# Performance work log

Measured on AMD Instinct MI355X. Metric: run time of the kernel, lower is better.

Reference implementation:

```python
import jax, jax.numpy as jnp
import numpy as np

N, E, D = 100000, 640000, 128


def _xavier(key, shape):
    return jax.random.normal(key, shape, jnp.float32) * np.float32(np.sqrt(2.0 / (shape[0] + shape[1])))


def setup_inputs() -> dict:
    key = jax.random.key(0)
    ks = jax.random.split(key, 16)
    inp = {
        "x": jax.random.normal(ks[0], (N, D), jnp.float32),
        "prompt_h": jax.random.normal(ks[1], (N, D), jnp.float32),
        "edge_attr": jax.random.normal(ks[2], (E, D), jnp.float32),
        "prompt_e": jax.random.normal(ks[3], (E, D), jnp.float32),
        "edge_index": jax.random.randint(ks[4], (2, E), 0, N, dtype=jnp.int32),
        # Linear weights stored [in, out] (torch stores [out, in]; math identical)
        "Wq": _xavier(ks[5], (D, D)), "bq": jnp.zeros((D,), jnp.float32),
        "Wk": _xavier(ks[6], (D, D)), "bk": jnp.zeros((D,), jnp.float32),
        "Wv": _xavier(ks[7], (D, D)), "bv": jnp.zeros((D,), jnp.float32),
        "We1": _xavier(ks[8], (D, D)), "be1": jnp.zeros((D,), jnp.float32),
        "We2": _xavier(ks[9], (D, D)), "be2": jnp.zeros((D,), jnp.float32),
        "Wh": _xavier(ks[10], (D, D)), "bh": jnp.zeros((D,), jnp.float32),
        "Wf1": _xavier(ks[11], (D, 2 * D)), "bf1": jnp.zeros((2 * D,), jnp.float32),
        "Wf2": _xavier(ks[12], (2 * D, D)), "bf2": jnp.zeros((D,), jnp.float32),
    }
    return inp


def reference(x, prompt_h, edge_attr, prompt_e, edge_index,
              Wq, bq, Wk, bk, Wv, bv, We1, be1, We2, be2,
              Wh, bh, Wf1, bf1, Wf2, bf2):
    relu = jax.nn.relu
    # Projections (dropout=0, eval mode)
    Q = x @ Wq + bq                      # [N, D]
    K = prompt_h @ Wk + bk               # [N, D]
    V = prompt_h @ Wv + bv               # [N, D]
    h = relu(Q * K)                      # attn_product='mul', score_act with relu
    # Edge-enhanced messages: gather source node scores per edge
    src = h[edge_index[0]]               # [E, D]
    e = relu((edge_attr + prompt_e) @ We1 + be1)
    e = relu((e + prompt_e) @ We2 + be2)  # updated edge_attr (update_e=True)
    msg = relu(src + e)                  # [E, D]
    # scatter-add aggregation into destination nodes
    aggr = jax.ops.segment_sum(msg, edge_index[1], num_segments=x.shape[0])  # [N, D]
    h_out = relu((h + V + aggr) @ Wh + bh)
    h_out = h_out + x                    # residual (in_dim == out_dim)
    h_out = relu(h_out @ Wf1 + bf1)
    h_out = h_out @ Wf2 + bf2            # [N, D]
    return h_out, e
```

## Files before the change

### kernel.cpp

```cpp
#include <hip/hip_runtime.h>

typedef __attribute__((ext_vector_type(8))) short bfrag;
typedef __attribute__((ext_vector_type(4))) float f4;

__device__ __forceinline__ unsigned short f2b(float f) {
  unsigned int u = __builtin_bit_cast(unsigned int, f);
  u = (u + 0x7fffu + ((u >> 16) & 1u)) >> 16;
  return (unsigned short)u;
}
__device__ __forceinline__ float b2f(unsigned short s) {
  unsigned int u = ((unsigned int)s) << 16;
  return __builtin_bit_cast(float, u);
}
__device__ __forceinline__ float relu(float v) { return v > 0.f ? v : 0.f; }

__device__ __forceinline__ void stage_A(char* dst, const float* s0, long r0, long maxRow) {
  const int tid = threadIdx.x;
#pragma unroll
  for (int i = 0; i < 4; ++i) {
    int ch = tid + (i << 8);
    int row = ch >> 4, kg = ch & 15;
    long gr = r0 + row;
    float v[8];
    if (gr < maxRow) {
      const float4* p = (const float4*)(s0 + gr * 128 + kg * 8);
      float4 a = p[0], b = p[1];
      v[0] = a.x; v[1] = a.y; v[2] = a.z; v[3] = a.w;
      v[4] = b.x; v[5] = b.y; v[6] = b.z; v[7] = b.w;
    } else {
#pragma unroll
      for (int j = 0; j < 8; ++j) v[j] = 0.f;
    }
    union { unsigned short h[8]; uint4 u; } pk;
#pragma unroll
    for (int j = 0; j < 8; ++j) pk.h[j] = f2b(v[j]);
    *(uint4*)(dst + (((row << 8) + (kg << 4)) ^ ((row & 7) << 4))) = pk.u;
  }
}

__device__ __forceinline__ void stage_A_mix(char* dst, const unsigned short* hb,
                                            const float* ag, long r0, long maxRow) {
  const int tid = threadIdx.x;
#pragma unroll
  for (int i = 0; i < 4; ++i) {
    int ch = tid + (i << 8);
    int row = ch >> 4, kg = ch & 15;
    long gr = r0 + row;
    union { unsigned short h[8]; uint4 u; } pk;
    if (gr < maxRow) {
      uint4 hv = *(const uint4*)(hb + gr * 128 + kg * 8);
      const float4* q = (const float4*)(ag + gr * 128 + kg * 8);
      float4 c = q[0], d = q[1];
      pk.h[0] = f2b(b2f((unsigned short)hv.x) + c.x);
      pk.h[1] = f2b(b2f((unsigned short)(hv.x >> 16)) + c.y);
      pk.h[2] = f2b(b2f((unsigned short)hv.y) + c.z);
      pk.h[3] = f2b(b2f((unsigned short)(hv.y >> 16)) + c.w);
      pk.h[4] = f2b(b2f((unsigned short)hv.z) + d.x);
      pk.h[5] = f2b(b2f((unsigned short)(hv.z >> 16)) + d.y);
      pk.h[6] = f2b(b2f((unsigned short)hv.w) + d.z);
      pk.h[7] = f2b(b2f((unsigned short)(hv.w >> 16)) + d.w);
    } else {
      pk.u = uint4{0, 0, 0, 0};
    }
    *(uint4*)(dst + (((row << 8) + (kg << 4)) ^ ((row & 7) << 4))) = pk.u;
  }
}

__device__ __forceinline__ void stage_W(char* dst, const unsigned short* src,
                                        int rowStride, int kOff) {
  const int tid = threadIdx.x;
#pragma unroll
  for (int i = 0; i < 8; ++i) {
    int ch = tid + (i << 8);
    int col = ch >> 4, kg = ch & 15;
    uint4 u = *(const uint4*)(src + (size_t)col * rowStride + kOff + kg * 8);
    *(uint4*)(dst + (((col << 8) + (kg << 4)) ^ ((col & 7) << 4))) = u;
  }
}

__device__ __forceinline__ void stage_Wh(char* dst, const unsigned short* src,
                                         int rowStride, int kOff) {
  const int tid = threadIdx.x;
#pragma unroll
  for (int i = 0; i < 4; ++i) {
    int ch = tid + (i << 8);
    int c = ch >> 3, kg = ch & 7;
    uint4 u = *(const uint4*)(src + (size_t)c * rowStride + kOff + kg * 8);
    *(uint4*)(dst + (((c << 7) + (kg << 4)) ^ ((c & 7) << 4))) = u;
  }
}

__device__ __forceinline__ void mm(const char* A, const char* W, int wm, int wn,
                                   int lane, f4 acc[2][4]) {
#pragma unroll
  for (int kk = 0; kk < 4; ++kk) {
    bfrag a[2], b[4];
#pragma unroll
    for (int rt = 0; rt < 2; ++rt) {
      int row = (wm << 5) + (rt << 4) + (lane & 15);
      a[rt] = *(const bfrag*)(A + (((row << 8) + (kk << 6) + ((lane >> 4) << 4)) ^ ((row & 7) << 4)));
    }
#pragma unroll
    for (int ct = 0; ct < 4; ++ct) {
      int col = (wn << 6) + (ct << 4) + (lane & 15);
      b[ct] = *(const bfrag*)(W + (((col << 8) + (kk << 6) + ((lane >> 4) << 4)) ^ ((col & 7) << 4)));
    }
#pragma unroll
    for (int rt = 0; rt < 2; ++rt)
#pragma unroll
      for (int ct = 0; ct < 4; ++ct)
        acc[rt][ct] = __builtin_amdgcn_mfma_f32_16x16x32_bf16(a[rt], b[ct], acc[rt][ct], 0, 0, 0);
  }
}

__device__ __forceinline__ void mm_h(const char* A, const char* W, int wm, int wn,
                                     int lane, f4 acc[2][4], int kh) {
#pragma unroll
  for (int kk2 = 0; kk2 < 2; ++kk2) {
    int kA = (kh << 1) + kk2;
    bfrag a[2], b[4];
#pragma unroll
    for (int rt = 0; rt < 2; ++rt) {
      int row = (wm << 5) + (rt << 4) + (lane & 15);
      a[rt] = *(const bfrag*)(A + (((row << 8) + (kA << 6) + ((lane >> 4) << 4)) ^ ((row & 7) << 4)));
    }
#pragma unroll
    for (int ct = 0; ct < 4; ++ct) {
      int col = (wn << 6) + (ct << 4) + (lane & 15);
      b[ct] = *(const bfrag*)(W + (((col << 7) + (kk2 << 6) + ((lane >> 4) << 4)) ^ ((col & 7) << 4)));
    }
#pragma unroll
    for (int rt = 0; rt < 2; ++rt)
#pragma unroll
      for (int ct = 0; ct < 4; ++ct)
        acc[rt][ct] = __builtin_amdgcn_mfma_f32_16x16x32_bf16(a[rt], b[ct], acc[rt][ct], 0, 0, 0);
  }
}

__device__ __forceinline__ void dump_half(char* Wl, const f4 acc[2][4], int lane, int wn) {
#pragma unroll
  for (int ct = 0; ct < 4; ++ct) {
    int col = (wn << 6) + (ct << 4) + (lane & 15);
#pragma unroll
    for (int rt = 0; rt < 2; ++rt)
#pragma unroll
      for (int j = 0; j < 4; ++j) {
        int lr = (rt << 4) + ((lane >> 4) << 2) + j;
        *(float*)(Wl + (((lr << 9) + (col << 2)) ^ ((lr & 7) << 4))) = acc[rt][ct][j];
      }
  }
}

__device__ __forceinline__ void dump_full(char* stg, const f4 acc[2][4], int lane, int wm, int wn) {
#pragma unroll
  for (int ct = 0; ct < 4; ++ct) {
    int col = (wn << 6) + (ct << 4) + (lane & 15);
#pragma unroll
    for (int rt = 0; rt < 2; ++rt)
#pragma unroll
      for (int j = 0; j < 4; ++j) {
        int rl = (wm << 5) + (rt << 4) + ((lane >> 4) << 2) + j;
        *(float*)(stg + (((rl << 9) + (col << 2)) ^ ((rl & 7) << 4))) = acc[rt][ct][j];
      }
  }
}

__global__ void k_prep(const float* __restrict__ Wq, const float* __restrict__ Wk,
                       const float* __restrict__ Wv, const float* __restrict__ We1,
                       const float* __restrict__ We2, const float* __restrict__ Wh,
                       const float* __restrict__ Wf1, const float* __restrict__ Wf2,
                       unsigned short* __restrict__ wt) {
  int b = blockIdx.x, t = threadIdx.x;
  if (b < 384) {
    int m = b >> 6;
    const float* tbl[6] = {Wq, Wk, Wv, We1, We2, Wh};
    const float* src = tbl[m];
    int local = ((b & 63) << 8) + t;
    int n = local >> 7, k = local & 127;
    wt[m * 16384 + local] = f2b(src[k * 128 + n]);
  } else if (b < 512) {
    int local = ((b - 384) << 8) + t;
    int n = local >> 7, k = local & 127;
    wt[98304 + local] = f2b(Wf1[k * 256 + n]);
  } else {
    int local = ((b - 512) << 8) + t;
    int n = local >> 8, k = local & 255;
    wt[131072 + local] = f2b(Wf2[k * 128 + n]);
  }
}

__global__ void k_deg(const int* __restrict__ ei, int* __restrict__ deg, long E) {
  long g = (long)blockIdx.x * 256 + threadIdx.x;
  if (g < E) atomicAdd(deg + ei[E + g], 1);
}

__global__ void k_scanA(const int* __restrict__ deg, int* __restrict__ ex,
                        int* __restrict__ bsum, int n) {
  __shared__ int s[256];
  int t = threadIdx.x; int g = blockIdx.x * 256 + t;
  int v = (g < n) ? deg[g] : 0;
  int val = v;
  s[t] = val; __syncthreads();
#pragma unroll
  for (int o = 1; o < 256; o <<= 1) {
    int u = (t >= o) ? s[t - o] : 0;
    __syncthreads();
    val += u; s[t] = val;
    __syncthreads();
  }
  if (g < n) ex[g] = val - v;
  if (t == 255) bsum[blockIdx.x] = val;
}

__global__ void k_scanB(int* __restrict__ bsum, int nb) {
  __shared__ int s[1024];
  int t = threadIdx.x;
  int v = (t < nb) ? bsum[t] : 0;
  int val = v;
  s[t] = val; __syncthreads();
#pragma unroll
  for (int o = 1; o < 1024; o <<= 1) {
    int u = (t >= o) ? s[t - o] : 0;
    __syncthreads();
    val += u; s[t] = val;
    __syncthreads();
  }
  if (t < nb) bsum[t] = val - v;
}

__global__ void k_scanC(const int* __restrict__ ex, const int* __restrict__ bsum,
                        int* __restrict__ off, int* __restrict__ cursor, int n) {
  int g = blockIdx.x * 256 + threadIdx.x;
  if (g < n) {
    int o = ex[g] + bsum[blockIdx.x];
    off[g] = o; cursor[g] = o;
  }
}

__global__ void k_fill(const int* __restrict__ ei, int* __restrict__ cursor,
                       int* __restrict__ eidx, long E) {
  long g = (long)blockIdx.x * 256 + threadIdx.x;
  if (g < E) {
    int pos = atomicAdd(cursor + ei[E + g], 1);
    eidx[pos] = (int)g;
  }
}

__global__ __launch_bounds__(256, 2) void k_nodes1(
    const float* __restrict__ x, const float* __restrict__ ph,
    const float* __restrict__ bq, const float* __restrict__ bk,
    const float* __restrict__ bv, const unsigned short* __restrict__ wt,
    unsigned short* __restrict__ hbf, unsigned short* __restrict__ hpvb, long N) {
  extern __shared__ char sm[];
  char* Ax = sm;
  char* Aph = sm + 16384;
  char* Wl = sm + 32768;
  long n0 = (long)blockIdx.x * 64;
  const int tid = threadIdx.x, lane = tid & 63, w = tid >> 6, wm = w >> 1, wn = w & 1;
  const int team = tid >> 5, c0 = (tid & 31) << 2;
  stage_A(Ax, x, n0, N);
  stage_A(Aph, ph, n0, N);
  stage_W(Wl, wt + 0, 128, 0);
  __syncthreads();
  f4 accQ[2][4] = {};
  mm(Ax, Wl, wm, wn, lane, accQ);
  __syncthreads();
  stage_W(Wl, wt + 16384, 128, 0);
  __syncthreads();
  f4 accK[2][4] = {};
  mm(Aph, Wl, wm, wn, lane, accK);
  __syncthreads();
  stage_W(Wl, wt + 32768, 128, 0);
  __syncthreads();
  f4 accV[2][4] = {};
  mm(Aph, Wl, wm, wn, lane, accV);
  __syncthreads();
#pragma unroll
  for (int ct = 0; ct < 4; ++ct) {
    int col = (wn << 6) + (ct << 4) + (lane & 15);
    float vbq = bq[col], vbk = bk[col], vbv = bv[col];
#pragma unroll
    for (int rt = 0; rt < 2; ++rt)
#pragma unroll
      for (int j = 0; j < 4; ++j) {
        int rl = (wm << 5) + (rt << 4) + ((lane >> 4) << 2) + j;
        float q = accQ[rt][ct][j] + vbq;
        float k = accK[rt][ct][j] + vbk;
        float v = accV[rt][ct][j] + vbv;
        float h = relu(q * k);
        *(unsigned short*)(Ax + (((rl << 8) + (col << 1)) ^ ((rl & 7) << 4))) = f2b(h);
        *(unsigned short*)(Aph + (((rl << 8) + (col << 1)) ^ ((rl & 7) << 4))) = f2b(h + v);
      }
  }
  __syncthreads();
#pragma unroll
  for (int it = 0; it < 8; ++it) {
    int r = team + (it << 3);
    long row = n0 + r;
    if (row < N) {
      uint2 hb = *(const uint2*)(Ax + (((r << 8) + (c0 << 1)) ^ ((r & 7) << 4)));
      uint2 hv = *(const uint2*)(Aph + (((r << 8) + (c0 << 1)) ^ ((r & 7) << 4)));
      *(uint2*)(hbf + row * 128 + c0) = hb;
      *(uint2*)(hpvb + row * 128 + c0) = hv;
    }
  }
}

__global__ __launch_bounds__(256, 3) void k_edges(
    const float* __restrict__ ea, const float* __restrict__ pe,
    const float* __restrict__ be1, const float* __restrict__ be2,
    const unsigned short* __restrict__ wt, const int* __restrict__ ei,
    const unsigned short* __restrict__ hbf, unsigned short* __restrict__ msg,
    float* __restrict__ eout, long E) {
  extern __shared__ char sm[];
  char* A = sm;
  unsigned short* peL = (unsigned short*)(sm + 16384);
  char* Wl = sm + 32768;
  char* stg = sm + 16384;
  const int tid = threadIdx.x;
  const int team = tid >> 5, c0 = (tid & 31) << 2;
  long e0 = (long)blockIdx.x * 64;

  uint2 hu[8];
#pragma unroll
  for (int it = 0; it < 8; ++it) {
    int r = team + (it << 3);
    long ge = e0 + r;
    int s = (ge < E) ? ei[ge] : 0;
    hu[it] = *(const uint2*)(hbf + (long)s * 128 + c0);
  }
#pragma unroll
  for (int i = 0; i < 4; ++i) {
    int ch = tid + (i << 8);
    int row = ch >> 4, kg = ch & 15;
    long gr = e0 + row;
    union { unsigned short h[8]; uint4 u; } s, q;
    if (gr < E) {
      const float4* pa = (const float4*)(ea + gr * 128 + kg * 8);
      const float4* pp = (const float4*)(pe + gr * 128 + kg * 8);
      float4 a0 = pa[0], a1 = pa[1];
      float4 p0 = pp[0], p1 = pp[1];
      s.h[0] = f2b(a0.x + p0.x); s.h[1] = f2b(a0.y + p0.y);
      s.h[2] = f2b(a0.z + p0.z); s.h[3] = f2b(a0.w + p0.w);
      s.h[4] = f2b(a1.x + p1.x); s.h[5] = f2b(a1.y + p1.y);
      s.h[6] = f2b(a1.z + p1.z); s.h[7] = f2b(a1.w + p1.w);
      q.h[0] = f2b(p0.x); q.h[1] = f2b(p0.y); q.h[2] = f2b(p0.z); q.h[3] = f2b(p0.w);
      q.h[4] = f2b(p1.x); q.h[5] = f2b(p1.y); q.h[6] = f2b(p1.z); q.h[7] = f2b(p1.w);
    } else {
      s.u = uint4{0, 0, 0, 0}; q.u = uint4{0, 0, 0, 0};
    }
    *(uint4*)((char*)peL + (row << 8) + (kg << 4)) = q.u;
    *(uint4*)(A + (((row << 8) + (kg << 4)) ^ ((row & 7) << 4))) = s.u;
  }
  stage_Wh(Wl, wt + 49152, 128, 0);
  __syncthreads();
  const int lane = tid & 63, w = tid >> 6, wm = w >> 1, wn = w & 1;
  f4 acc[2][4] = {};
  mm_h(A, Wl, wm, wn, lane, acc, 0);
  __syncthreads();
  stage_Wh(Wl, wt + 49152, 128, 64);
  __syncthreads();
  mm_h(A, Wl, wm, wn, lane, acc, 1);
  __syncthreads();
  const float4 vb1 = *(const float4*)(be1 + c0);
#pragma unroll
  for (int h = 0; h < 2; ++h) {
    if (wm == h) dump_half(Wl, acc, lane, wn);
    __syncthreads();
#pragma unroll
    for (int it = 0; it < 4; ++it) {
      int lr = team + (it << 3);
      int r = (h << 5) + lr;
      f4 a = *(const f4*)(Wl + (((lr << 9) + (c0 << 2)) ^ ((lr & 7) << 4)));
      uint2 pu = *(const uint2*)(peL + (r << 7) + c0);
      float p0 = b2f((unsigned short)pu.x), p1 = b2f((unsigned short)(pu.x >> 16));
      float p2 = b2f((unsigned short)pu.y), p3 = b2f((unsigned short)(pu.y >> 16));
      unsigned short t0 = f2b(relu(a[0] + vb1.x) + p0);
      unsigned short t1 = f2b(relu(a[1] + vb1.y) + p1);
      unsigned short t2 = f2b(relu(a[2] + vb1.z) + p2);
      unsigned short t3 = f2b(relu(a[3] + vb1.w) + p3);
      uint2 op;
      op.x = (unsigned int)t0 | ((unsigned int)t1 << 16);
      op.y = (unsigned int)t2 | ((unsigned int)t3 << 16);
      *(uint2*)(A + (((r << 8) + (c0 << 1)) ^ ((r & 7) << 4))) = op;
    }
    __syncthreads();
  }
  stage_Wh(Wl, wt + 65536, 128, 0);
  __syncthreads();
  f4 acc2[2][4] = {};
  mm_h(A, Wl, wm, wn, lane, acc2, 0);
  __syncthreads();
  stage_Wh(Wl, wt + 65536, 128, 64);
  __syncthreads();
  mm_h(A, Wl, wm, wn, lane, acc2, 1);
  __syncthreads();
  dump_full(stg, acc2, lane, wm, wn);
  __syncthreads();
  const float4 vb2 = *(const float4*)(be2 + c0);
#pragma unroll
  for (int it = 0; it < 8; ++it) {
    int r = team + (it << 3);
    long edge = e0 + r;
    if (edge < E) {
      f4 a = *(const f4*)(stg + (((r << 9) + (c0 << 2)) ^ ((r & 7) << 4)));
      float ev0 = relu(a[0] + vb2.x), ev1 = relu(a[1] + vb2.y);
      float ev2 = relu(a[2] + vb2.z), ev3 = relu(a[3] + vb2.w);
      float4 ov; ov.x = ev0; ov.y = ev1; ov.z = ev2; ov.w = ev3;
      *(float4*)(eout + edge * 128 + c0) = ov;
      float h0 = b2f((unsigned short)hu[it].x), h1 = b2f((unsigned short)(hu[it].x >> 16));
      float h2 = b2f((unsigned short)hu[it].y), h3 = b2f((unsigned short)(hu[it].y >> 16));
      unsigned short m0 = f2b(relu(ev0 + h0)), m1 = f2b(relu(ev1 + h1));
      unsigned short m2 = f2b(relu(ev2 + h2)), m3 = f2b(relu(ev3 + h3));
      uint2 mo;
      mo.x = (unsigned int)m0 | ((unsigned int)m1 << 16);
      mo.y = (unsigned int)m2 | ((unsigned int)m3 << 16);
      *(uint2*)(msg + edge * 128 + c0) = mo;
    }
  }
}

__global__ __launch_bounds__(256) void k_aggr(
    const int* __restrict__ off, const int* __restrict__ deg,
    const int* __restrict__ eidx, const unsigned short* __restrict__ msg,
    float* __restrict__ aggr, long N) {
  long node = (long)blockIdx.x * 4 + (threadIdx.x >> 6);
  if (node >= N) return;
  const int lane = threadIdx.x & 63;
  int st = off[node], d = deg[node];
  float a0 = 0.f, a1 = 0.f;
  int i = 0;
  for (; i + 3 < d; i += 4) {
    int e0i = eidx[st + i], e1i = eidx[st + i + 1];
    int e2i = eidx[st + i + 2], e3i = eidx[st + i + 3];
    unsigned int u0 = *(const unsigned int*)(msg + (long)e0i * 128 + lane * 2);
    unsigned int u1 = *(const unsigned int*)(msg + (long)e1i * 128 + lane * 2);
    unsigned int u2 = *(const unsigned int*)(msg + (long)e2i * 128 + lane * 2);
    unsigned int u3 = *(const unsigned int*)(msg + (long)e3i * 128 + lane * 2);
    a0 += b2f((unsigned short)u0) + b2f((unsigned short)u1) +
          b2f((unsigned short)u2) + b2f((unsigned short)u3);
    a1 += b2f((unsigned short)(u0 >> 16)) + b2f((unsigned short)(u1 >> 16)) +
          b2f((unsigned short)(u2 >> 16)) + b2f((unsigned short)(u3 >> 16));
  }
  for (; i < d; ++i) {
    int eid = eidx[st + i];
    unsigned int u = *(const unsigned int*)(msg + (long)eid * 128 + lane * 2);
    a0 += b2f((unsigned short)u);
    a1 += b2f((unsigned short)(u >> 16));
  }
  *(float2*)(aggr + node * 128 + lane * 2) = float2{a0, a1};
}

__global__ __launch_bounds__(256, 2) void k_nodes2(
    const unsigned short* __restrict__ hpvb, const float* __restrict__ aggr,
    const float* __restrict__ x, const float* __restrict__ bh,
    const float* __restrict__ bf1, const float* __restrict__ bf2,
    const unsigned short* __restrict__ wt, float* __restrict__ out, long N) {
  extern __shared__ char sm[];
  char* A = sm;
  char* T = sm + 16384;
  char* Wl = sm + 32768;
  long n0 = (long)blockIdx.x * 64;
  const int tid = threadIdx.x;
  stage_A_mix(A, hpvb, aggr, n0, N);
  stage_W(Wl, wt + 81920, 128, 0);
  __syncthreads();
  const int lane = tid & 63, w = tid >> 6, wm = w >> 1, wn = w & 1;
  f4 acc1[2][4] = {};
  mm(A, Wl, wm, wn, lane, acc1);
  __syncthreads();
#pragma unroll
  for (int ct = 0; ct < 4; ++ct) {
    int col = (wn << 6) + (ct << 4) + (lane & 15);
    float bb = bh[col];
#pragma unroll
    for (int rt = 0; rt < 2; ++rt)
#pragma unroll
      for (int j = 0; j < 4; ++j) {
        int rl = (wm << 5) + (rt << 4) + ((lane >> 4) << 2) + j;
        long row = n0 + rl;
        float xv = (row < N) ? x[row * 128 + col] : 0.f;
        float tv = relu(acc1[rt][ct][j] + bb) + xv;
        *(unsigned short*)(T + (((rl << 8) + (col << 1)) ^ ((rl & 7) << 4))) = f2b(tv);
      }
  }
  stage_W(Wl, wt + 98304, 128, 0);
  __syncthreads();
  f4 accA[2][4] = {};
  mm(T, Wl, wm, wn, lane, accA);
  __syncthreads();
#pragma unroll
  for (int ct = 0; ct < 4; ++ct) {
    int col = (wn << 6) + (ct << 4) + (lane & 15);
    float bb = bf1[col];
#pragma unroll
    for (int rt = 0; rt < 2; ++rt)
#pragma unroll
      for (int j = 0; j < 4; ++j) {
        int rl = (wm << 5) + (rt << 4) + ((lane >> 4) << 2) + j;
        float uv = relu(accA[rt][ct][j] + bb);
        *(unsigned short*)(A + (((rl << 8) + (col << 1)) ^ ((rl & 7) << 4))) = f2b(uv);
      }
  }
  stage_W(Wl, wt + 131072, 256, 0);
  __syncthreads();
  f4 acc3[2][4] = {};
  mm(A, Wl, wm, wn, lane, acc3);
  __syncthreads();
  stage_W(Wl, wt + 114688, 128, 0);
  __syncthreads();
  f4 accB[2][4] = {};
  mm(T, Wl, wm, wn, lane, accB);
  __syncthreads();
#pragma unroll
  for (int ct = 0; ct < 4; ++ct) {
    int col = (wn << 6) + (ct << 4) + (lane & 15);
    float bb = bf1[128 + col];
#pragma unroll
    for (int rt = 0; rt < 2; ++rt)
#pragma unroll
      for (int j = 0; j < 4; ++j) {
        int rl = (wm << 5) + (rt << 4) + ((lane >> 4) << 2) + j;
        float uv = relu(accB[rt][ct][j] + bb);
        *(unsigned short*)(A + (((rl << 8) + (col << 1)) ^ ((rl & 7) << 4))) = f2b(uv);
      }
  }
  stage_W(Wl, wt + 131072, 256, 128);
  __syncthreads();
  mm(A, Wl, wm, wn, lane, acc3);
#pragma unroll
  for (int ct = 0; ct < 4; ++ct) {
    int col = (wn << 6) + (ct << 4) + (lane & 15);
    float bb = bf2[col];
#pragma unroll
    for (int rt = 0; rt < 2; ++rt)
#pragma unroll
      for (int j = 0; j < 4; ++j) {
        int rl = (wm << 5) + (rt << 4) + ((lane >> 4) << 2) + j;
        long row = n0 + rl;
        if (row < N) out[row * 128 + col] = acc3[rt][ct][j] + bb;
      }
  }
}

extern "C" void kernel_launch(void* const* d_in, const int* in_sizes, int n_in,
                              void* d_out, int out_size, void* d_ws, size_t ws_size,
                              hipStream_t stream) {
  const float* x   = (const float*)d_in[0];
  const float* ph  = (const float*)d_in[1];
  const float* ea  = (const float*)d_in[2];
  const float* pe  = (const float*)d_in[3];
  const int*   ei  = (const int*)d_in[4];
  const float* Wq  = (const float*)d_in[5];  const float* bq  = (const float*)d_in[6];
  const float* Wk  = (const float*)d_in[7];  const float* bk  = (const float*)d_in[8];
  const float* Wv  = (const float*)d_in[9];  const float* bv  = (const float*)d_in[10];
  const float* We1 = (const float*)d_in[11]; const float* be1 = (const float*)d_in[12];
  const float* We2 = (const float*)d_in[13]; const float* be2 = (const float*)d_in[14];
  const float* Wh  = (const float*)d_in[15]; const float* bh  = (const float*)d_in[16];
  const float* Wf1 = (const float*)d_in[17]; const float* bf1 = (const float*)d_in[18];
  const float* Wf2 = (const float*)d_in[19]; const float* bf2 = (const float*)d_in[20];
  const long N = in_sizes[0] / 128;
  const long E = in_sizes[2] / 128;

  char* ws = (char*)d_ws;
  size_t pos_ = 0;
  auto alloc = [&](size_t bytes) { size_t p = pos_; pos_ += (bytes + 255) & ~255ULL; return p; };
  size_t o_wt   = alloc(327680);
  size_t o_hbf  = alloc((size_t)N * 256);
  size_t o_hpv  = alloc((size_t)N * 256);
  size_t o_aggr = alloc((size_t)N * 512);
  size_t o_deg  = alloc((size_t)N * 4);
  size_t o_ex   = alloc((size_t)N * 4);
  size_t o_cur  = alloc((size_t)N * 4);
  size_t o_off  = alloc((size_t)N * 4);
  size_t o_bsum = alloc(4096);
  size_t o_eidx = alloc((size_t)E * 4);
  size_t o_msg  = alloc((size_t)E * 256);
  (void)pos_;

  unsigned short* wt   = (unsigned short*)(ws + o_wt);
  unsigned short* hbf  = (unsigned short*)(ws + o_hbf);
  unsigned short* hpvb = (unsigned short*)(ws + o_hpv);
  float* aggr = (float*)(ws + o_aggr);
  float* outH = (float*)d_out;
  float* outE = outH + N * 128;

  k_prep<<<640, 256, 0, stream>>>(Wq, Wk, Wv, We1, We2, Wh, Wf1, Wf2, wt);
  int nb = (int)((N + 63) / 64);
  int eb = (int)((E + 63) / 64);
  k_nodes1<<<nb, 256, 65536, stream>>>(x, ph, bq, bk, bv, wt, hbf, hpvb, N);

  int* deg = (int*)(ws + o_deg);
  int* ex  = (int*)(ws + o_ex);
  int* cur = (int*)(ws + o_cur);
  int* off = (int*)(ws + o_off);
  int* bsum = (int*)(ws + o_bsum);
  int* eidx = (int*)(ws + o_eidx);
  unsigned short* msg = (unsigned short*)(ws + o_msg);
  int nb1 = (int)((N + 255) / 256);
  hipMemsetAsync(deg, 0, (size_t)N * 4, stream);
  k_deg<<<(int)((E + 255) / 256), 256, 0, stream>>>(ei, deg, E);
  k_scanA<<<nb1, 256, 0, stream>>>(deg, ex, bsum, (int)N);
  k_scanB<<<1, 1024, 0, stream>>>(bsum, nb1);
  k_scanC<<<nb1, 256, 0, stream>>>(ex, bsum, off, cur, (int)N);
  k_fill<<<(int)((E + 255) / 256), 256, 0, stream>>>(ei, cur, eidx, E);
  k_edges<<<eb, 256, 49152, stream>>>(ea, pe, be1, be2, wt, ei, hbf, msg, outE, E);
  k_aggr<<<(int)((N + 3) / 4), 256, 0, stream>>>(off, deg, eidx, msg, aggr, N);
  k_nodes2<<<nb, 256, 65536, stream>>>(hpvb, aggr, x, bh, bf1, bf2, wt, outH, N);
}
```

Baseline: 582.4 us.

## Fuse CSR aggregation into node MLP kernel and defer source-row gather in edge kernel

Removes the separate k_aggr kernel and its fp32 aggr buffer. k_nodes2 now gathers messages per destination node directly into its shared-memory A tile, adding the h+V term before bf16 packing. The residual x is prestaged into shared memory as bf16 instead of read from global in the epilogue. In k_edges, source indices go to shared memory and the hbf gather moves to the epilogue instead of being held in registers across the GEMMs. This lowers register pressure and global traffic, but the fused gather may serialize latency inside the GEMM kernel, and x is now rounded to bf16.

Result: no change. 591.6 us (+1.6%).

```diff
diff --git a/kernel.cpp b/kernel.cpp
--- a/kernel.cpp
+++ b/kernel.cpp
@@ -34,34 +34,6 @@
     union { unsigned short h[8]; uint4 u; } pk;
 #pragma unroll
     for (int j = 0; j < 8; ++j) pk.h[j] = f2b(v[j]);
-    *(uint4*)(dst + (((row << 8) + (kg << 4)) ^ ((row & 7) << 4))) = pk.u;
-  }
-}
-
-__device__ __forceinline__ void stage_A_mix(char* dst, const unsigned short* hb,
-                                            const float* ag, long r0, long maxRow) {
-  const int tid = threadIdx.x;
-#pragma unroll
-  for (int i = 0; i < 4; ++i) {
-    int ch = tid + (i << 8);
-    int row = ch >> 4, kg = ch & 15;
-    long gr = r0 + row;
-    union { unsigned short h[8]; uint4 u; } pk;
-    if (gr < maxRow) {
-      uint4 hv = *(const uint4*)(hb + gr * 128 + kg * 8);
-      const float4* q = (const float4*)(ag + gr * 128 + kg * 8);
-      float4 c = q[0], d = q[1];
-      pk.h[0] = f2b(b2f((unsigned short)hv.x) + c.x);
-      pk.h[1] = f2b(b2f((unsigned short)(hv.x >> 16)) + c.y);
-      pk.h[2] = f2b(b2f((unsigned short)hv.y) + c.z);
-      pk.h[3] = f2b(b2f((unsigned short)(hv.y >> 16)) + c.w);
-      pk.h[4] = f2b(b2f((unsigned short)hv.z) + d.x);
-      pk.h[5] = f2b(b2f((unsigned short)(hv.z >> 16)) + d.y);
-      pk.h[6] = f2b(b2f((unsigned short)hv.w) + d.z);
-      pk.h[7] = f2b(b2f((unsigned short)(hv.w >> 16)) + d.w);
-    } else {
-      pk.u = uint4{0, 0, 0, 0};
-    }
     *(uint4*)(dst + (((row << 8) + (kg << 4)) ^ ((row & 7) << 4))) = pk.u;
   }
 }
@@ -317,18 +289,11 @@
   unsigned short* peL = (unsigned short*)(sm + 16384);
   char* Wl = sm + 32768;
   char* stg = sm + 16384;
+  int* srcI = (int*)(sm + 49152);
   const int tid = threadIdx.x;
   const int team = tid >> 5, c0 = (tid & 31) << 2;
   long e0 = (long)blockIdx.x * 64;
-
-  uint2 hu[8];
-#pragma unroll
-  for (int it = 0; it < 8; ++it) {
-    int r = team + (it << 3);
-    long ge = e0 + r;
-    int s = (ge < E) ? ei[ge] : 0;
-    hu[it] = *(const uint2*)(hbf + (long)s * 128 + c0);
-  }
+  if (tid < 64) srcI[tid] = (e0 + tid < E) ? ei[e0 + tid] : 0;
 #pragma unroll
   for (int i = 0; i < 4; ++i) {
     int ch = tid + (i << 8);
@@ -408,8 +373,9 @@
       float ev2 = relu(a[2] + vb2.z), ev3 = relu(a[3] + vb2.w);
       float4 ov; ov.x = ev0; ov.y = ev1; ov.z = ev2; ov.w = ev3;
       *(float4*)(eout + edge * 128 + c0) = ov;
-      float h0 = b2f((unsigned short)hu[it].x), h1 = b2f((unsigned short)(hu[it].x >> 16));
-      float h2 = b2f((unsigned short)hu[it].y), h3 = b2f((unsigned short)(hu[it].y >> 16));
+      uint2 hu = *(const uint2*)(hbf + (long)srcI[r] * 128 + c0);
+      float h0 = b2f((unsigned short)hu.x), h1 = b2f((unsigned short)(hu.x >> 16));
+      float h2 = b2f((unsigned short)hu.y), h3 = b2f((unsigned short)(hu.y >> 16));
       unsigned short m0 = f2b(relu(ev0 + h0)), m1 = f2b(relu(ev1 + h1));
       unsigned short m2 = f2b(relu(ev2 + h2)), m3 = f2b(relu(ev3 + h3));
       uint2 mo;
@@ -420,39 +386,10 @@
   }
 }
 
-__global__ __launch_bounds__(256) void k_aggr(
+__global__ __launch_bounds__(256, 2) void k_nodes2(
+    const unsigned short* __restrict__ hpvb,
     const int* __restrict__ off, const int* __restrict__ deg,
     const int* __restrict__ eidx, const unsigned short* __restrict__ msg,
-    float* __restrict__ aggr, long N) {
-  long node = (long)blockIdx.x * 4 + (threadIdx.x >> 6);
-  if (node >= N) return;
-  const int lane = threadIdx.x & 63;
-  int st = off[node], d = deg[node];
-  float a0 = 0.f, a1 = 0.f;
-  int i = 0;
-  for (; i + 3 < d; i += 4) {
-    int e0i = eidx[st + i], e1i = eidx[st + i + 1];
-    int e2i = eidx[st + i + 2], e3i = eidx[st + i + 3];
-    unsigned int u0 = *(const unsigned int*)(msg + (long)e0i * 128 + lane * 2);
-    unsigned int u1 = *(const unsigned int*)(msg + (long)e1i * 128 + lane * 2);
-    unsigned int u2 = *(const unsigned int*)(msg + (long)e2i * 128 + lane * 2);
-    unsigned int u3 = *(const unsigned int*)(msg + (long)e3i * 128 + lane * 2);
-    a0 += b2f((unsigned short)u0) + b2f((unsigned short)u1) +
-          b2f((unsigned short)u2) + b2f((unsigned short)u3);
-    a1 += b2f((unsigned short)(u0 >> 16)) + b2f((unsigned short)(u1 >> 16)) +
-          b2f((unsigned short)(u2 >> 16)) + b2f((unsigned short)(u3 >> 16));
-  }
-  for (; i < d; ++i) {
-    int eid = eidx[st + i];
-    unsigned int u = *(const unsigned int*)(msg + (long)eid * 128 + lane * 2);
-    a0 += b2f((unsigned short)u);
-    a1 += b2f((unsigned short)(u >> 16));
-  }
-  *(float2*)(aggr + node * 128 + lane * 2) = float2{a0, a1};
-}
-
-__global__ __launch_bounds__(256, 2) void k_nodes2(
-    const unsigned short* __restrict__ hpvb, const float* __restrict__ aggr,
     const float* __restrict__ x, const float* __restrict__ bh,
     const float* __restrict__ bf1, const float* __restrict__ bf2,
     const unsigned short* __restrict__ wt, float* __restrict__ out, long N) {
@@ -462,7 +399,43 @@
   char* Wl = sm + 32768;
   long n0 = (long)blockIdx.x * 64;
   const int tid = threadIdx.x;
-  stage_A_mix(A, hpvb, aggr, n0, N);
+  const int team = tid >> 5, c0 = (tid & 31) << 2;
+  stage_A(T, x, n0, N);
+#pragma unroll
+  for (int it = 0; it < 8; ++it) {
+    int r = team + (it << 3);
+    long node = n0 + r;
+    float s0 = 0.f, s1 = 0.f, s2 = 0.f, s3 = 0.f;
+    if (node < N) {
+      uint2 hv = *(const uint2*)(hpvb + node * 128 + c0);
+      s0 = b2f((unsigned short)hv.x);
+      s1 = b2f((unsigned short)(hv.x >> 16));
+      s2 = b2f((unsigned short)hv.y);
+      s3 = b2f((unsigned short)(hv.y >> 16));
+      int o = off[node], d = deg[node];
+      int i = 0;
+      for (; i + 1 < d; i += 2) {
+        int ea0 = eidx[o + i], ea1 = eidx[o + i + 1];
+        uint2 m0 = *(const uint2*)(msg + (long)ea0 * 128 + c0);
+        uint2 m1 = *(const uint2*)(msg + (long)ea1 * 128 + c0);
+        s0 += b2f((unsigned short)m0.x) + b2f((unsigned short)m1.x);
+        s1 += b2f((unsigned short)(m0.x >> 16)) + b2f((unsigned short)(m1.x >> 16));
+        s2 += b2f((unsigned short)m0.y) + b2f((unsigned short)m1.y);
+        s3 += b2f((unsigned short)(m0.y >> 16)) + b2f((unsigned short)(m1.y >> 16));
+      }
+      if (i < d) {
+        uint2 m0 = *(const uint2*)(msg + (long)eidx[o + i] * 128 + c0);
+        s0 += b2f((unsigned short)m0.x);
+        s1 += b2f((unsigned short)(m0.x >> 16));
+        s2 += b2f((unsigned short)m0.y);
+        s3 += b2f((unsigned short)(m0.y >> 16));
+      }
+    }
+    uint2 pk;
+    pk.x = (unsigned)f2b(s0) | ((unsigned)f2b(s1) << 16);
+    pk.y = (unsigned)f2b(s2) | ((unsigned)f2b(s3) << 16);
+    *(uint2*)(A + (((r << 8) + (c0 << 1)) ^ ((r & 7) << 4))) = pk;
+  }
   stage_W(Wl, wt + 81920, 128, 0);
   __syncthreads();
   const int lane = tid & 63, w = tid >> 6, wm = w >> 1, wn = w & 1;
@@ -478,10 +451,11 @@
 #pragma unroll
       for (int j = 0; j < 4; ++j) {
         int rl = (wm << 5) + (rt << 4) + ((lane >> 4) << 2) + j;
-        long row = n0 + rl;
-        float xv = (row < N) ? x[row * 128 + col] : 0.f;
+        unsigned short* slot =
+            (unsigned short*)(T + (((rl << 8) + (col << 1)) ^ ((rl & 7) << 4)));
+        float xv = b2f(*slot);
         float tv = relu(acc1[rt][ct][j] + bb) + xv;
-        *(unsigned short*)(T + (((rl << 8) + (col << 1)) ^ ((rl & 7) << 4))) = f2b(tv);
+        *slot = f2b(tv);
       }
   }
   stage_W(Wl, wt + 98304, 128, 0);
@@ -568,7 +542,6 @@
   size_t o_wt   = alloc(327680);
   size_t o_hbf  = alloc((size_t)N * 256);
   size_t o_hpv  = alloc((size_t)N * 256);
-  size_t o_aggr = alloc((size_t)N * 512);
   size_t o_deg  = alloc((size_t)N * 4);
   size_t o_ex   = alloc((size_t)N * 4);
   size_t o_cur  = alloc((size_t)N * 4);
@@ -581,7 +554,6 @@
   unsigned short* wt   = (unsigned short*)(ws + o_wt);
   unsigned short* hbf  = (unsigned short*)(ws + o_hbf);
   unsigned short* hpvb = (unsigned short*)(ws + o_hpv);
-  float* aggr = (float*)(ws + o_aggr);
   float* outH = (float*)d_out;
   float* outE = outH + N * 128;
 
@@ -604,7 +576,6 @@
   k_scanB<<<1, 1024, 0, stream>>>(bsum, nb1);
   k_scanC<<<nb1, 256, 0, stream>>>(ex, bsum, off, cur, (int)N);
   k_fill<<<(int)((E + 255) / 256), 256, 0, stream>>>(ei, cur, eidx, E);
-  k_edges<<<eb, 256, 49152, stream>>>(ea, pe, be1, be2, wt, ei, hbf, msg, outE, E);
-  k_aggr<<<(int)((N + 3) / 4), 256, 0, stream>>>(off, deg, eidx, msg, aggr, N);
-  k_nodes2<<<nb, 256, 65536, stream>>>(hpvb, aggr, x, bh, bf1, bf2, wt, outH, N);
-}
+  k_edges<<<eb, 256, 49408, stream>>>(ea, pe, be1, be2, wt, ei, hbf, msg, outE, E);
+  k_nodes2<<<nb, 256, 65536, stream>>>(hpvb, off, deg, eidx, msg, x, bh, bf1, bf2, wt, outH, N);
+}
```

## Shrink k_edges LDS footprint and registers to raise occupancy

Applied to the files above, without the earlier changes.

Keeps the bf16 prompt_e values in registers instead of an LDS buffer, stages ea/pe with a per-team row mapping matching the epilogue, and defers the gathered source-node row load to the epilogue using indices cached in LDS. Shared memory drops from 48KB to about 33KB and launch bounds rise to 4 blocks per CU, with the aim of better latency hiding in the edge kernel. In exchange, the gather latency is no longer hidden behind the GEMMs, and the per-thread loads become narrower float4 accesses.

Result: slower. 798.8 us (+37.2%).

```diff
diff --git a/kernel.cpp b/kernel.cpp
--- a/kernel.cpp
+++ b/kernel.cpp
@@ -306,7 +306,7 @@
   }
 }
 
-__global__ __launch_bounds__(256, 3) void k_edges(
+__global__ __launch_bounds__(256, 4) void k_edges(
     const float* __restrict__ ea, const float* __restrict__ pe,
     const float* __restrict__ be1, const float* __restrict__ be2,
     const unsigned short* __restrict__ wt, const int* __restrict__ ei,
@@ -314,43 +314,30 @@
     float* __restrict__ eout, long E) {
   extern __shared__ char sm[];
   char* A = sm;
-  unsigned short* peL = (unsigned short*)(sm + 16384);
-  char* Wl = sm + 32768;
-  char* stg = sm + 16384;
+  char* Wl = sm + 16384;
+  char* stg = sm;
+  int* srcI = (int*)(sm + 32768);
   const int tid = threadIdx.x;
   const int team = tid >> 5, c0 = (tid & 31) << 2;
   long e0 = (long)blockIdx.x * 64;
-
-  uint2 hu[8];
+  if (tid < 64) srcI[tid] = (e0 + tid < E) ? ei[e0 + tid] : 0;
+
+  uint2 peR[8];
 #pragma unroll
   for (int it = 0; it < 8; ++it) {
     int r = team + (it << 3);
     long ge = e0 + r;
-    int s = (ge < E) ? ei[ge] : 0;
-    hu[it] = *(const uint2*)(hbf + (long)s * 128 + c0);
-  }
-#pragma unroll
-  for (int i = 0; i < 4; ++i) {
-    int ch = tid + (i << 8);
-    int row = ch >> 4, kg = ch & 15;
-    long gr = e0 + row;
-    union { unsigned short h[8]; uint4 u; } s, q;
-    if (gr < E) {
-      const float4* pa = (const float4*)(ea + gr * 128 + kg * 8);
-      const float4* pp = (const float4*)(pe + gr * 128 + kg * 8);
-      float4 a0 = pa[0], a1 = pa[1];
-      float4 p0 = pp[0], p1 = pp[1];
-      s.h[0] = f2b(a0.x + p0.x); s.h[1] = f2b(a0.y + p0.y);
-      s.h[2] = f2b(a0.z + p0.z); s.h[3] = f2b(a0.w + p0.w);
-      s.h[4] = f2b(a1.x + p1.x); s.h[5] = f2b(a1.y + p1.y);
-      s.h[6] = f2b(a1.z + p1.z); s.h[7] = f2b(a1.w + p1.w);
-      q.h[0] = f2b(p0.x); q.h[1] = f2b(p0.y); q.h[2] = f2b(p0.z); q.h[3] = f2b(p0.w);
-      q.h[4] = f2b(p1.x); q.h[5] = f2b(p1.y); q.h[6] = f2b(p1.z); q.h[7] = f2b(p1.w);
-    } else {
-      s.u = uint4{0, 0, 0, 0}; q.u = uint4{0, 0, 0, 0};
-    }
-    *(uint4*)((char*)peL + (row << 8) + (kg << 4)) = q.u;
-    *(uint4*)(A + (((row << 8) + (kg << 4)) ^ ((row & 7) << 4))) = s.u;
+    float4 av = make_float4(0.f, 0.f, 0.f, 0.f), pv = av;
+    if (ge < E) {
+      av = *(const float4*)(ea + ge * 128 + c0);
+      pv = *(const float4*)(pe + ge * 128 + c0);
+    }
+    peR[it].x = (unsigned)f2b(pv.x) | ((unsigned)f2b(pv.y) << 16);
+    peR[it].y = (unsigned)f2b(pv.z) | ((unsigned)f2b(pv.w) << 16);
+    uint2 s;
+    s.x = (unsigned)f2b(av.x + pv.x) | ((unsigned)f2b(av.y + pv.y) << 16);
+    s.y = (unsigned)f2b(av.z + pv.z) | ((unsigned)f2b(av.w + pv.w) << 16);
+    *(uint2*)(A + (((r << 8) + (c0 << 1)) ^ ((r & 7) << 4))) = s;
   }
   stage_Wh(Wl, wt + 49152, 128, 0);
   __syncthreads();
@@ -371,17 +358,17 @@
     for (int it = 0; it < 4; ++it) {
       int lr = team + (it << 3);
       int r = (h << 5) + lr;
+      int j = (h << 2) + it;
       f4 a = *(const f4*)(Wl + (((lr << 9) + (c0 << 2)) ^ ((lr & 7) << 4)));
-      uint2 pu = *(const uint2*)(peL + (r << 7) + c0);
-      float p0 = b2f((unsigned short)pu.x), p1 = b2f((unsigned short)(pu.x >> 16));
-      float p2 = b2f((unsigned short)pu.y), p3 = b2f((unsigned short)(pu.y >> 16));
-      unsigned short t0 = f2b(relu(a[0] + vb1.x) + p0);
-      unsigned short t1 = f2b(relu(a[1] + vb1.y) + p1);
-      unsigned short t2 = f2b(relu(a[2] + vb1.z) + p2);
-      unsigned short t3 = f2b(relu(a[3] + vb1.w) + p3);
+      float p0 = b2f((unsigned short)peR[j].x), p1 = b2f((unsigned short)(peR[j].x >> 16));
+      float p2 = b2f((unsigned short)peR[j].y), p3 = b2f((unsigned short)(peR[j].y >> 16));
+      float t0 = relu(a[0] + vb1.x) + p0;
+      float t1 = relu(a[1] + vb1.y) + p1;
+      float t2 = relu(a[2] + vb1.z) + p2;
+      float t3 = relu(a[3] + vb1.w) + p3;
       uint2 op;
-      op.x = (unsigned int)t0 | ((unsigned int)t1 << 16);
-      op.y = (unsigned int)t2 | ((unsigned int)t3 << 16);
+      op.x = (unsigned)f2b(t0) | ((unsigned)f2b(t1) << 16);
+      op.y = (unsigned)f2b(t2) | ((unsigned)f2b(t3) << 16);
       *(uint2*)(A + (((r << 8) + (c0 << 1)) ^ ((r & 7) << 4))) = op;
     }
     __syncthreads();
@@ -408,8 +395,9 @@
       float ev2 = relu(a[2] + vb2.z), ev3 = relu(a[3] + vb2.w);
       float4 ov; ov.x = ev0; ov.y = ev1; ov.z = ev2; ov.w = ev3;
       *(float4*)(eout + edge * 128 + c0) = ov;
-      float h0 = b2f((unsigned short)hu[it].x), h1 = b2f((unsigned short)(hu[it].x >> 16));
-      float h2 = b2f((unsigned short)hu[it].y), h3 = b2f((unsigned short)(hu[it].y >> 16));
+      uint2 hu = *(const uint2*)(hbf + (long)srcI[r] * 128 + c0);
+      float h0 = b2f((unsigned short)hu.x), h1 = b2f((unsigned short)(hu.x >> 16));
+      float h2 = b2f((unsigned short)hu.y), h3 = b2f((unsigned short)(hu.y >> 16));
       unsigned short m0 = f2b(relu(ev0 + h0)), m1 = f2b(relu(ev1 + h1));
       unsigned short m2 = f2b(relu(ev2 + h2)), m3 = f2b(relu(ev3 + h3));
       uint2 mo;
@@ -604,7 +592,7 @@
   k_scanB<<<1, 1024, 0, stream>>>(bsum, nb1);
   k_scanC<<<nb1, 256, 0, stream>>>(ex, bsum, off, cur, (int)N);
   k_fill<<<(int)((E + 255) / 256), 256, 0, stream>>>(ei, cur, eidx, E);
-  k_edges<<<eb, 256, 49152, stream>>>(ea, pe, be1, be2, wt, ei, hbf, msg, outE, E);
+  k_edges<<<eb, 256, 33024, stream>>>(ea, pe, be1, be2, wt, ei, hbf, msg, outE, E);
   k_aggr<<<(int)((N + 3) / 4), 256, 0, stream>>>(off, deg, eidx, msg, aggr, N);
   k_nodes2<<<nb, 256, 65536, stream>>>(hpvb, aggr, x, bh, bf1, bf2, wt, outH, N);
 }
```
